# Kernel tuning notes

Hardware: AMD Instinct MI355X
Metric: run time of the kernel (lower is better)

The kernel has to match this reference:

```python
import jax, jax.numpy as jnp
import numpy as np

N = 50000      # nodes
E = 800000     # edges (avg degree 16)
IN = 128       # input feature dim
HID = 32       # per-head hidden dim
H = 4          # attention heads
C = 40         # num classes
SLOPE = 0.2    # leaky relu negative slope


def setup_inputs() -> dict:
    key = jax.random.key(0)
    ks = jax.random.split(key, 14)
    s = 0.05
    inputs = jax.random.normal(ks[0], (N, IN), jnp.float32)
    target = jax.random.normal(ks[1], (N, IN), jnp.float32)
    lamb = jax.random.uniform(ks[2], (1,), jnp.float32)
    src = jax.random.randint(ks[3], (E,), 0, N, jnp.int32)
    dst = jax.random.randint(ks[4], (E,), 0, N, jnp.int32)
    W0 = jax.random.normal(ks[5], (IN, H * HID), jnp.float32) * s
    al0 = jax.random.normal(ks[6], (H, HID), jnp.float32) * s
    ar0 = jax.random.normal(ks[7], (H, HID), jnp.float32) * s
    W1 = jax.random.normal(ks[8], (H * HID, H * HID), jnp.float32) * s
    al1 = jax.random.normal(ks[9], (H, HID), jnp.float32) * s
    ar1 = jax.random.normal(ks[10], (H, HID), jnp.float32) * s
    Wout = jax.random.normal(ks[11], (H * HID, C), jnp.float32) * s
    bout = jnp.zeros((C,), jnp.float32)
    return dict(inputs=inputs, target=target, lamb=lamb,
                W0=W0, al0=al0, ar0=ar0, W1=W1, al1=al1, ar1=ar1,
                Wout=Wout, bout=bout, src=src, dst=dst)


def gat_conv(h, W, al, ar, src, dst, residual):
    # h: [N, in_dim]; W: [in_dim, H*HID]; al/ar: [H, HID]
    feat = (h @ W).reshape(N, H, HID)                  # [N,H,D]
    el = jnp.einsum('nhd,hd->nh', feat, al)            # [N,H]
    er = jnp.einsum('nhd,hd->nh', feat, ar)            # [N,H]
    e = jax.nn.leaky_relu(el[src] + er[dst], SLOPE)    # [E,H]
    # edge softmax over incoming edges of each dst node
    emax = jax.ops.segment_max(e, dst, num_segments=N)  # [N,H]
    ee = jnp.exp(e - emax[dst])                          # [E,H]
    denom = jax.ops.segment_sum(ee, dst, num_segments=N)
    a = ee / denom[dst]                                  # [E,H]
    msg = feat[src] * a[:, :, None]                      # [E,H,D]
    out = jax.ops.segment_sum(msg, dst, num_segments=N)  # [N,H,D]
    if residual:
        out = out + h.reshape(N, H, HID)  # identity residual (in == H*HID)
    return jax.nn.elu(out)


def reference(inputs, target, lamb, W0, al0, ar0, W1, al1, ar1, Wout, bout, src, dst):
    def path(x):
        h = gat_conv(x, W0, al0, ar0, src, dst, residual=False).reshape(N, H * HID)
        h = gat_conv(h, W1, al1, ar1, src, dst, residual=True).reshape(N, H * HID)
        return h

    h = path(inputs)
    h2 = path(target)
    lam = lamb[0]
    h = lam * h + (1.0 - lam) * h2   # mixup_hidden=True
    logits = h @ Wout + bout
    return (h, logits)
```

## Files before the change

### kernel.cpp

```cpp
#include <hip/hip_runtime.h>
#include <hip/hip_bf16.h>
#include <cstddef>

#define GN 50000
#define GE 800000
#define GH 4
#define GD 32
#define SLOPE 0.2f
#define LOG2E 1.4426950408889634f

typedef unsigned short ushort_t;
typedef unsigned int uint_t;
using short8 = __attribute__((ext_vector_type(8))) short;
using float4v = __attribute__((ext_vector_type(4))) float;

__device__ __forceinline__ ushort_t f2bf(float f) {
    union { float f; uint_t u; } v; v.f = f;
    uint_t r = v.u + 0x7fff + ((v.u >> 16) & 1);
    return (ushort_t)(r >> 16);
}
__device__ __forceinline__ float bflo(uint_t u) { return __uint_as_float(u << 16); }
__device__ __forceinline__ float bfhi(uint_t u) { return __uint_as_float(u & 0xffff0000u); }
__device__ __forceinline__ float bfu(ushort_t u) { return __uint_as_float((uint_t)u << 16); }

__device__ __forceinline__ uint_t cvt_pk_bf16(float lo, float hi) {
    uint_t r;
    asm("v_cvt_pk_bf16_f32 %0, %1, %2" : "=v"(r) : "v"(lo), "v"(hi));
    return r;
}

#if __has_builtin(__builtin_amdgcn_exp2f)
#define EXP2F(x) __builtin_amdgcn_exp2f(x)
#else
#define EXP2F(x) exp2f(x)
#endif

__device__ __forceinline__ int slotmap(int a) {
    return (a < GN) ? (a << 1) : (((a - GN) << 1) | 1);
}

__global__ void k_hist(const int* __restrict__ dst, int* __restrict__ deg, int E) {
    int i = blockIdx.x * 256 + threadIdx.x;
    if (i < E) atomicAdd(&deg[dst[i]], 1);
}

__global__ void k_scan1(const int* __restrict__ deg, int* __restrict__ row_ptr,
                        int* __restrict__ partials, int n) {
    __shared__ int s[256];
    int t = threadIdx.x;
    int i = blockIdx.x * 256 + t;
    int v = (i < n) ? deg[i] : 0;
    s[t] = v;
    __syncthreads();
    for (int off = 1; off < 256; off <<= 1) {
        int add = (t >= off) ? s[t - off] : 0;
        __syncthreads();
        s[t] += add;
        __syncthreads();
    }
    if (i < n) row_ptr[i] = s[t] - v;
    if (t == 255) partials[blockIdx.x] = s[255];
}

__global__ void k_scan2(int* __restrict__ partials, int nb) {
    __shared__ int s[256];
    int t = threadIdx.x;
    int v = (t < nb) ? partials[t] : 0;
    s[t] = v;
    __syncthreads();
    for (int off = 1; off < 256; off <<= 1) {
        int add = (t >= off) ? s[t - off] : 0;
        __syncthreads();
        s[t] += add;
        __syncthreads();
    }
    if (t < nb) partials[t] = s[t] - v;
}

__global__ void k_scan3(int* __restrict__ row_ptr, int* __restrict__ wpos,
                        const int* __restrict__ partials, int n, int E) {
    int i = blockIdx.x * 256 + threadIdx.x;
    if (i < n) {
        int rp = row_ptr[i] + partials[i >> 8];
        row_ptr[i] = rp;
        wpos[i] = rp;
        if (i == 0) row_ptr[n] = E;
    }
}

__global__ void k_fill(const int* __restrict__ src, const int* __restrict__ dst,
                       int* __restrict__ wpos, int* __restrict__ csr_src, int E) {
    int i = blockIdx.x * 256 + threadIdx.x;
    if (i < E) {
        int p = atomicAdd(&wpos[dst[i]], 1);
        csr_src[p] = src[i];
    }
}

__global__ void k_cvt_all(const float* __restrict__ W0, const float* __restrict__ W1,
                          const float* __restrict__ Wout,
                          ushort_t* __restrict__ wbt, ushort_t* __restrict__ woutb) {
    int t = blockIdx.x * 256 + threadIdx.x;
    if (t < 32768) {
        int m = t >> 14;
        int o = t & 16383;
        int n = o >> 7, k = o & 127;
        const float* W = m ? W1 : W0;
        wbt[t] = f2bf(W[k * 128 + n]);
    } else {
        int u = t - 32768;
        if (u < 48 * 128) {
            int n = u >> 7, k = u & 127;
            float w = (n < 40) ? Wout[k * 40 + n] : 0.f;
            ushort_t h = f2bf(w);
            woutb[u] = h;
            woutb[48 * 128 + u] = f2bf(w - bfu(h));
        }
    }
}

__device__ __forceinline__ void lr_epilogue(const float4v acc[2][8],
                                            const float* __restrict__ ar,
                                            float* __restrict__ er,
                                            int r0, int quad, int col, int M) {
#pragma unroll
    for (int rt = 0; rt < 2; rt++) {
#pragma unroll
        for (int h = 0; h < 4; h++) {
            float arv0 = ar[h * 32 + col], arv1 = ar[h * 32 + 16 + col];
            float pr[4];
#pragma unroll
            for (int r = 0; r < 4; r++)
                pr[r] = acc[rt][2 * h][r] * arv0 + acc[rt][2 * h + 1][r] * arv1;
#pragma unroll
            for (int m = 1; m < 16; m <<= 1) {
#pragma unroll
                for (int r = 0; r < 4; r++) pr[r] += __shfl_xor(pr[r], m, 64);
            }
            if (col == 8 + h) {
#pragma unroll
                for (int r = 0; r < 4; r++) {
                    int row = r0 + rt * 16 + quad * 4 + r;
                    if (row < M) er[slotmap(row) * 4 + h] = pr[r] * LOG2E;
                }
            }
        }
    }
}

__device__ __forceinline__ void store_c_bf16(ushort_t* __restrict__ Cb,
                                             const float4v acc[2][8],
                                             int r0, int quad, int col, int M) {
#pragma unroll
    for (int rt = 0; rt < 2; rt++)
#pragma unroll
        for (int nt = 0; nt < 8; nt++) {
            int rb = r0 + rt * 16 + quad * 4;
            int c = nt * 16 + col;
            uint_t p01 = cvt_pk_bf16(acc[rt][nt][0], acc[rt][nt][1]);
            uint_t p23 = cvt_pk_bf16(acc[rt][nt][2], acc[rt][nt][3]);
            if (rb + 0 < M) Cb[(size_t)slotmap(rb + 0) * 128 + c] = (ushort_t)p01;
            if (rb + 1 < M) Cb[(size_t)slotmap(rb + 1) * 128 + c] = (ushort_t)(p01 >> 16);
            if (rb + 2 < M) Cb[(size_t)slotmap(rb + 2) * 128 + c] = (ushort_t)p23;
            if (rb + 3 < M) Cb[(size_t)slotmap(rb + 3) * 128 + c] = (ushort_t)(p23 >> 16);
        }
}

__global__ __launch_bounds__(256) void gemm_mfma32(const float* __restrict__ A0,
                                                   const float* __restrict__ A1,
                                                   const ushort_t* __restrict__ WbT,
                                                   const float* __restrict__ ar,
                                                   ushort_t* __restrict__ Cb,
                                                   float* __restrict__ er, int M) {
    __shared__ ushort_t Bs[128][136];
    int tid = threadIdx.x;
    for (int i = tid; i < 128 * 16; i += 256) {
        int n = i >> 4;
        int kc = (i & 15) << 3;
        *(short8*)&Bs[n][kc] = *(const short8*)&WbT[n * 128 + kc];
    }
    __syncthreads();
    int wid = tid >> 6, lane = tid & 63;
    int r0 = blockIdx.x * 128 + wid * 32;
    int col = lane & 15, quad = lane >> 4;
    float4v acc[2][8];
#pragma unroll
    for (int rt = 0; rt < 2; rt++)
#pragma unroll
        for (int t = 0; t < 8; t++) acc[rt][t] = (float4v){0.f, 0.f, 0.f, 0.f};
    int ar_[2] = {r0 + col, r0 + 16 + col};
    const float* Ap[2];
#pragma unroll
    for (int rt = 0; rt < 2; rt++) {
        int a = ar_[rt];
        Ap[rt] = (a < M) ? ((a < GN) ? (A0 + (size_t)a * 128)
                                     : (A1 + (size_t)(a - GN) * 128)) : nullptr;
    }
#pragma unroll
    for (int ks = 0; ks < 4; ks++) {
        short8 af[2];
#pragma unroll
        for (int rt = 0; rt < 2; rt++) {
            af[rt] = (short8){};
            if (Ap[rt]) {
                float4 v0 = *(const float4*)&Ap[rt][ks * 32 + quad * 8];
                float4 v1 = *(const float4*)&Ap[rt][ks * 32 + quad * 8 + 4];
                union { short8 s; uint_t u[4]; } cv;
                cv.u[0] = cvt_pk_bf16(v0.x, v0.y);
                cv.u[1] = cvt_pk_bf16(v0.z, v0.w);
                cv.u[2] = cvt_pk_bf16(v1.x, v1.y);
                cv.u[3] = cvt_pk_bf16(v1.z, v1.w);
                af[rt] = cv.s;
            }
        }
#pragma unroll
        for (int nt = 0; nt < 8; nt++) {
            short8 bf = *(const short8*)&Bs[nt * 16 + col][ks * 32 + quad * 8];
            acc[0][nt] = __builtin_amdgcn_mfma_f32_16x16x32_bf16(af[0], bf, acc[0][nt], 0, 0, 0);
            acc[1][nt] = __builtin_amdgcn_mfma_f32_16x16x32_bf16(af[1], bf, acc[1][nt], 0, 0, 0);
        }
    }
    store_c_bf16(Cb, acc, r0, quad, col, M);
    lr_epilogue(acc, ar, er, r0, quad, col, M);
}

__global__ __launch_bounds__(256) void gemm_mfma(const ushort_t* __restrict__ A,
                                                 const ushort_t* __restrict__ WbT,
                                                 const float* __restrict__ ar,
                                                 ushort_t* __restrict__ Cb,
                                                 float* __restrict__ er, int M) {
    __shared__ ushort_t Bs[128][136];
    int tid = threadIdx.x;
    for (int i = tid; i < 128 * 16; i += 256) {
        int n = i >> 4;
        int kc = (i & 15) << 3;
        *(short8*)&Bs[n][kc] = *(const short8*)&WbT[n * 128 + kc];
    }
    __syncthreads();
    int wid = tid >> 6, lane = tid & 63;
    int r0 = blockIdx.x * 128 + wid * 32;
    int col = lane & 15, quad = lane >> 4;
    float4v acc[2][8];
#pragma unroll
    for (int rt = 0; rt < 2; rt++)
#pragma unroll
        for (int t = 0; t < 8; t++) acc[rt][t] = (float4v){0.f, 0.f, 0.f, 0.f};
    int ar_[2] = {r0 + col, r0 + 16 + col};
    const ushort_t* Ap[2];
#pragma unroll
    for (int rt = 0; rt < 2; rt++) {
        int a = ar_[rt];
        Ap[rt] = (a < M) ? (A + (size_t)slotmap(a) * 128) : nullptr;
    }
#pragma unroll
    for (int ks = 0; ks < 4; ks++) {
        short8 af[2];
#pragma unroll
        for (int rt = 0; rt < 2; rt++) {
            af[rt] = (short8){};
            if (Ap[rt]) af[rt] = *(const short8*)&Ap[rt][ks * 32 + quad * 8];
        }
#pragma unroll
        for (int nt = 0; nt < 8; nt++) {
            short8 bf = *(const short8*)&Bs[nt * 16 + col][ks * 32 + quad * 8];
            acc[0][nt] = __builtin_amdgcn_mfma_f32_16x16x32_bf16(af[0], bf, acc[0][nt], 0, 0, 0);
            acc[1][nt] = __builtin_amdgcn_mfma_f32_16x16x32_bf16(af[1], bf, acc[1][nt], 0, 0, 0);
        }
    }
    store_c_bf16(Cb, acc, r0, quad, col, M);
    lr_epilogue(acc, ar, er, r0, quad, col, M);
}

__device__ __forceinline__ void agg_core(
    const ushort_t* __restrict__ featb, float4 alv, float ern,
    const int* __restrict__ csr_src, int base, int deg, uint_t fofs,
    float& v0, float& v1, float& v2, float& v3) {
    if (deg <= 0) { v0 = v1 = v2 = v3 = 0.f; return; }
    float a0 = 0.f, a1 = 0.f, a2 = 0.f, a3 = 0.f, ss = 0.f;
    int nblk = (deg + 15) >> 4;
    int jb = base;
    int r1 = deg - 1;
    int s[16], t[16];
#pragma unroll
    for (int k = 0; k < 16; k++) s[k] = csr_src[jb + min(k, r1)];
    int b = 0;
    for (;;) {
        int rem = deg - (b << 4);
        uint2 f[16];
#pragma unroll
        for (int k = 0; k < 16; k++)
            f[k] = *(const uint2*)&featb[(uint_t)s[k] * 256u + fofs];
        bool more = (b + 1) < nblk;
        if (more) {
            int nj = jb + 16;
            int r2 = rem - 17;
#pragma unroll
            for (int k = 0; k < 16; k++) t[k] = csr_src[nj + min(k, r2)];
        }
#pragma unroll
        for (int k = 0; k < 16; k++) {
            float x0 = bflo(f[k].x), x1 = bfhi(f[k].x);
            float x2 = bflo(f[k].y), x3 = bfhi(f[k].y);
            float d = x0 * alv.x + x1 * alv.y + x2 * alv.z + x3 * alv.w;
            d += __shfl_xor(d, 1, 64);
            d += __shfl_xor(d, 2, 64);
            d += __shfl_xor(d, 4, 64);
            float e = d + ern;
            e = fmaxf(e, SLOPE * e);
            float w = (k < rem) ? EXP2F(e) : 0.f;
            ss += w;
            a0 += w * x0; a1 += w * x1; a2 += w * x2; a3 += w * x3;
        }
        if (!more) break;
        b++; jb += 16;
#pragma unroll
        for (int k = 0; k < 16; k++) s[k] = t[k];
    }
    float inv = 1.f / ss;
    v0 = a0 * inv; v1 = a1 * inv; v2 = a2 * inv; v3 = a3 * inv;
}

__global__ __launch_bounds__(512) void gat_agg_l1(
    const ushort_t* __restrict__ featb, const float* __restrict__ al,
    const float* __restrict__ er, const int* __restrict__ row_ptr,
    const int* __restrict__ csr_src, ushort_t* __restrict__ abuf) {
    int n = __builtin_amdgcn_readfirstlane(blockIdx.x * 8 + (threadIdx.x >> 6));
    if (n >= GN) return;
    int lane = threadIdx.x & 63;
    int half = lane >> 5;
    int q = lane & 31;
    int head = (lane >> 3) & 3, j8 = lane & 7, q4 = q << 2;
    float4 alv = *(const float4*)&al[head * 32 + j8 * 4];
    alv.x *= LOG2E; alv.y *= LOG2E; alv.z *= LOG2E; alv.w *= LOG2E;
    uint_t fofs = (uint_t)(half * 128 + q4);
    float ern = er[(uint_t)n * 8u + (uint_t)(half * 4 + head)];
    int base = row_ptr[n];
    int deg = row_ptr[n + 1] - base;
    float v0, v1, v2, v3;
    agg_core(featb, alv, ern, csr_src, base, deg, fofs, v0, v1, v2, v3);
    v0 = v0 > 0.f ? v0 : __expf(v0) - 1.f;
    v1 = v1 > 0.f ? v1 : __expf(v1) - 1.f;
    v2 = v2 > 0.f ? v2 : __expf(v2) - 1.f;
    v3 = v3 > 0.f ? v3 : __expf(v3) - 1.f;
    size_t idx = ((size_t)(2 * n + half)) * 128 + q4;
    uint2 o;
    o.x = cvt_pk_bf16(v0, v1);
    o.y = cvt_pk_bf16(v2, v3);
    *(uint2*)&abuf[idx] = o;
}

__global__ __launch_bounds__(512) void gat_agg_l2(
    const ushort_t* __restrict__ featb, const float* __restrict__ al,
    const float* __restrict__ er, const int* __restrict__ row_ptr,
    const int* __restrict__ csr_src, const ushort_t* __restrict__ resid,
    const float* __restrict__ lamb, float* __restrict__ outh) {
    int tid = threadIdx.x;
    int n = __builtin_amdgcn_readfirstlane(blockIdx.x * 8 + (tid >> 6));
    if (n >= GN) return;
    int lane = tid & 63;
    int half = lane >> 5;
    int q = lane & 31;
    int head = (lane >> 3) & 3, j8 = lane & 7, q4 = q << 2;
    float4 alv = *(const float4*)&al[head * 32 + j8 * 4];
    alv.x *= LOG2E; alv.y *= LOG2E; alv.z *= LOG2E; alv.w *= LOG2E;
    uint_t fofs = (uint_t)(half * 128 + q4);
    float ern = er[(uint_t)n * 8u + (uint_t)(half * 4 + head)];
    int base = row_ptr[n];
    int deg = row_ptr[n + 1] - base;
    float v0, v1, v2, v3;
    agg_core(featb, alv, ern, csr_src, base, deg, fofs, v0, v1, v2, v3);
    size_t idx = ((size_t)(2 * n + half)) * 128 + q4;
    ushort4 r = *(const ushort4*)&resid[idx];
    v0 += bfu(r.x); v1 += bfu(r.y); v2 += bfu(r.z); v3 += bfu(r.w);
    v0 = v0 > 0.f ? v0 : __expf(v0) - 1.f;
    v1 = v1 > 0.f ? v1 : __expf(v1) - 1.f;
    v2 = v2 > 0.f ? v2 : __expf(v2) - 1.f;
    v3 = v3 > 0.f ? v3 : __expf(v3) - 1.f;
    float p0 = __shfl_xor(v0, 32, 64);
    float p1 = __shfl_xor(v1, 32, 64);
    float p2 = __shfl_xor(v2, 32, 64);
    float p3 = __shfl_xor(v3, 32, 64);
    float lam = lamb[0];
    if (half == 0) {
        float m0 = lam * v0 + (1.f - lam) * p0;
        float m1 = lam * v1 + (1.f - lam) * p1;
        float m2 = lam * v2 + (1.f - lam) * p2;
        float m3 = lam * v3 + (1.f - lam) * p3;
        *(float4*)&outh[(size_t)n * 128 + q4] = make_float4(m0, m1, m2, m3);
    }
}

__global__ __launch_bounds__(256) void k_logits(const float* __restrict__ Hf,
                                                const ushort_t* __restrict__ Wb,
                                                const float* __restrict__ bout,
                                                float* __restrict__ outlog) {
    __shared__ ushort_t Bh[48][136];
    __shared__ ushort_t Bl[48][136];
    int tid = threadIdx.x;
    for (int i = tid; i < 48 * 16; i += 256) {
        int n = i >> 4;
        int kc = (i & 15) << 3;
        *(short8*)&Bh[n][kc] = *(const short8*)&Wb[n * 128 + kc];
        *(short8*)&Bl[n][kc] = *(const short8*)&Wb[48 * 128 + n * 128 + kc];
    }
    __syncthreads();
    int wid = tid >> 6, lane = tid & 63;
    int r0 = blockIdx.x * 128 + wid * 32;
    int col = lane & 15, quad = lane >> 4;
    float4v acc[2][3];
#pragma unroll
    for (int rt = 0; rt < 2; rt++)
#pragma unroll
        for (int nt = 0; nt < 3; nt++) acc[rt][nt] = (float4v){0.f, 0.f, 0.f, 0.f};
    int ar_[2] = {r0 + col, r0 + 16 + col};
#pragma unroll
    for (int ks = 0; ks < 4; ks++) {
        short8 ah[2], alo[2];
#pragma unroll
        for (int rt = 0; rt < 2; rt++) {
            ah[rt] = (short8){};
            alo[rt] = (short8){};
            if (ar_[rt] < GN) {
                const float* p = Hf + (size_t)ar_[rt] * 128 + ks * 32 + quad * 8;
                float4 x = *(const float4*)p;
                float4 y = *(const float4*)(p + 4);
                union { short8 s; uint_t u[4]; } ch, cl;
                ch.u[0] = cvt_pk_bf16(x.x, x.y);
                ch.u[1] = cvt_pk_bf16(x.z, x.w);
                ch.u[2] = cvt_pk_bf16(y.x, y.y);
                ch.u[3] = cvt_pk_bf16(y.z, y.w);
                cl.u[0] = cvt_pk_bf16(x.x - bflo(ch.u[0]), x.y - bfhi(ch.u[0]));
                cl.u[1] = cvt_pk_bf16(x.z - bflo(ch.u[1]), x.w - bfhi(ch.u[1]));
                cl.u[2] = cvt_pk_bf16(y.x - bflo(ch.u[2]), y.y - bfhi(ch.u[2]));
                cl.u[3] = cvt_pk_bf16(y.z - bflo(ch.u[3]), y.w - bfhi(ch.u[3]));
                ah[rt] = ch.s;
                alo[rt] = cl.s;
            }
        }
#pragma unroll
        for (int nt = 0; nt < 3; nt++) {
            short8 bh = *(const short8*)&Bh[nt * 16 + col][ks * 32 + quad * 8];
            short8 bl = *(const short8*)&Bl[nt * 16 + col][ks * 32 + quad * 8];
#pragma unroll
            for (int rt = 0; rt < 2; rt++) {
                acc[rt][nt] = __builtin_amdgcn_mfma_f32_16x16x32_bf16(ah[rt], bh, acc[rt][nt], 0, 0, 0);
                acc[rt][nt] = __builtin_amdgcn_mfma_f32_16x16x32_bf16(alo[rt], bh, acc[rt][nt], 0, 0, 0);
                acc[rt][nt] = __builtin_amdgcn_mfma_f32_16x16x32_bf16(ah[rt], bl, acc[rt][nt], 0, 0, 0);
            }
        }
    }
#pragma unroll
    for (int nt = 0; nt < 3; nt++) {
        int c = nt * 16 + col;
        if (c < 40) {
            float bv = bout[c];
#pragma unroll
            for (int rt = 0; rt < 2; rt++)
#pragma unroll
                for (int r = 0; r < 4; r++) {
                    int row = r0 + rt * 16 + quad * 4 + r;
                    if (row < GN) outlog[(size_t)row * 40 + c] = acc[rt][nt][r] + bv;
                }
        }
    }
}

extern "C" void kernel_launch(void* const* d_in, const int* in_sizes, int n_in,
                              void* d_out, int out_size, void* d_ws, size_t ws_size,
                              hipStream_t stream) {
    const float* inputs = (const float*)d_in[0];
    const float* target = (const float*)d_in[1];
    const float* lamb   = (const float*)d_in[2];
    const float* W0     = (const float*)d_in[3];
    const float* al0    = (const float*)d_in[4];
    const float* ar0    = (const float*)d_in[5];
    const float* W1     = (const float*)d_in[6];
    const float* al1    = (const float*)d_in[7];
    const float* ar1    = (const float*)d_in[8];
    const float* Wout   = (const float*)d_in[9];
    const float* bout   = (const float*)d_in[10];
    const int*   src    = (const int*)d_in[11];
    const int*   dst    = (const int*)d_in[12];

    float* out = (float*)d_out;
    float* outh = out;
    float* outlog = out + (size_t)GN * 128;

    const int NP = 2 * GN;
    ushort_t* featb = (ushort_t*)d_ws;
    ushort_t* abuf  = featb + (size_t)NP * 128;
    float* er = (float*)(abuf + (size_t)NP * 128);
    ushort_t* wbt = (ushort_t*)(er + (size_t)NP * GH);
    int* row_ptr  = (int*)(wbt + 2 * 128 * 128);
    int* wpos     = row_ptr + (GN + 1);
    int* csr_src  = wpos + GN;
    int* partials = csr_src + GE + 16;
    ushort_t* woutb = (ushort_t*)(partials + 256);

    const int nb = (GN + 255) / 256;
    const int eb = (GE + 255) / 256;
    const int gblocks = (NP + 127) / 128;
    const int aggblocks = (GN + 7) / 8;
    const int lblocks = (GN + 127) / 128;

    hipMemsetAsync(wpos, 0, GN * sizeof(int), stream);
    k_hist<<<eb, 256, 0, stream>>>(dst, wpos, GE);
    k_scan1<<<nb, 256, 0, stream>>>(wpos, row_ptr, partials, GN);
    k_scan2<<<1, 256, 0, stream>>>(partials, nb);
    k_scan3<<<nb, 256, 0, stream>>>(row_ptr, wpos, partials, GN, GE);
    k_fill<<<eb, 256, 0, stream>>>(src, dst, wpos, csr_src, GE);

    k_cvt_all<<<152, 256, 0, stream>>>(W0, W1, Wout, wbt, woutb);

    gemm_mfma32<<<gblocks, 256, 0, stream>>>(inputs, target, wbt, ar0,
                                             featb, er, NP);
    gat_agg_l1<<<aggblocks, 512, 0, stream>>>(featb, al0, er, row_ptr, csr_src, abuf);

    gemm_mfma<<<gblocks, 256, 0, stream>>>(abuf, wbt + 128 * 128, ar1,
                                           featb, er, NP);
    gat_agg_l2<<<aggblocks, 512, 0, stream>>>(featb, al1, er, row_ptr, csr_src,
                                              abuf, lamb, outh);

    k_logits<<<lblocks, 256, 0, stream>>>(outh, woutb, bout, outlog);
}
```

Before: 396.5 us.

## Precompute el in GEMM epilogue and stream edges across eight nodes per wave

The GEMM epilogue now also computes the left attention scores el per node, so aggregation reads a precomputed scalar per edge instead of recomputing a 32-wide dot product with shuffles for every edge. The aggregation kernel is rewritten so each wave walks a contiguous run of edges covering eight destination nodes in fixed windows of eight. A new per-edge csr_dst array supplies the destination index, and edge weights are spread across lanes with ds_swizzle. This is meant to cut per-edge ALU and shuffle work and the padding waste of low-degree nodes, in exchange for an extra el buffer, the csr_dst writes and more complex control flow at node boundaries.

```diff
diff --git a/kernel.cpp b/kernel.cpp
--- a/kernel.cpp
+++ b/kernel.cpp
@@ -34,6 +34,8 @@
 #else
 #define EXP2F(x) exp2f(x)
 #endif
+
+#define SWZ_B(v, imm) __uint_as_float((uint_t)__builtin_amdgcn_ds_swizzle((int)__float_as_uint(v), (imm)))
 
 __device__ __forceinline__ int slotmap(int a) {
     return (a < GN) ? (a << 1) : (((a - GN) << 1) | 1);
@@ -89,11 +91,14 @@
 }
 
 __global__ void k_fill(const int* __restrict__ src, const int* __restrict__ dst,
-                       int* __restrict__ wpos, int* __restrict__ csr_src, int E) {
+                       int* __restrict__ wpos, int* __restrict__ csr_src,
+                       ushort_t* __restrict__ csr_dst, int E) {
     int i = blockIdx.x * 256 + threadIdx.x;
     if (i < E) {
-        int p = atomicAdd(&wpos[dst[i]], 1);
+        int d = dst[i];
+        int p = atomicAdd(&wpos[d], 1);
         csr_src[p] = src[i];
+        csr_dst[p] = (ushort_t)d;
     }
 }
 
@@ -120,22 +125,37 @@
 }
 
 __device__ __forceinline__ void lr_epilogue(const float4v acc[2][8],
+                                            const float* __restrict__ al,
                                             const float* __restrict__ ar,
+                                            float* __restrict__ el,
                                             float* __restrict__ er,
                                             int r0, int quad, int col, int M) {
 #pragma unroll
     for (int rt = 0; rt < 2; rt++) {
 #pragma unroll
         for (int h = 0; h < 4; h++) {
+            float alv0 = al[h * 32 + col], alv1 = al[h * 32 + 16 + col];
             float arv0 = ar[h * 32 + col], arv1 = ar[h * 32 + 16 + col];
-            float pr[4];
-#pragma unroll
-            for (int r = 0; r < 4; r++)
+            float pl[4], pr[4];
+#pragma unroll
+            for (int r = 0; r < 4; r++) {
+                pl[r] = acc[rt][2 * h][r] * alv0 + acc[rt][2 * h + 1][r] * alv1;
                 pr[r] = acc[rt][2 * h][r] * arv0 + acc[rt][2 * h + 1][r] * arv1;
+            }
 #pragma unroll
             for (int m = 1; m < 16; m <<= 1) {
 #pragma unroll
-                for (int r = 0; r < 4; r++) pr[r] += __shfl_xor(pr[r], m, 64);
+                for (int r = 0; r < 4; r++) {
+                    pl[r] += __shfl_xor(pl[r], m, 64);
+                    pr[r] += __shfl_xor(pr[r], m, 64);
+                }
+            }
+            if (col == h) {
+#pragma unroll
+                for (int r = 0; r < 4; r++) {
+                    int row = r0 + rt * 16 + quad * 4 + r;
+                    if (row < M) el[slotmap(row) * 4 + h] = pl[r] * LOG2E;
+                }
             }
             if (col == 8 + h) {
 #pragma unroll
@@ -169,8 +189,10 @@
 __global__ __launch_bounds__(256) void gemm_mfma32(const float* __restrict__ A0,
                                                    const float* __restrict__ A1,
                                                    const ushort_t* __restrict__ WbT,
+                                                   const float* __restrict__ al,
                                                    const float* __restrict__ ar,
                                                    ushort_t* __restrict__ Cb,
+                                                   float* __restrict__ el,
                                                    float* __restrict__ er, int M) {
     __shared__ ushort_t Bs[128][136];
     int tid = threadIdx.x;
@@ -221,13 +243,15 @@
         }
     }
     store_c_bf16(Cb, acc, r0, quad, col, M);
-    lr_epilogue(acc, ar, er, r0, quad, col, M);
+    lr_epilogue(acc, al, ar, el, er, r0, quad, col, M);
 }
 
 __global__ __launch_bounds__(256) void gemm_mfma(const ushort_t* __restrict__ A,
                                                  const ushort_t* __restrict__ WbT,
+                                                 const float* __restrict__ al,
                                                  const float* __restrict__ ar,
                                                  ushort_t* __restrict__ Cb,
+                                                 float* __restrict__ el,
                                                  float* __restrict__ er, int M) {
     __shared__ ushort_t Bs[128][136];
     int tid = threadIdx.x;
@@ -268,125 +292,142 @@
         }
     }
     store_c_bf16(Cb, acc, r0, quad, col, M);
-    lr_epilogue(acc, ar, er, r0, quad, col, M);
-}
-
-__device__ __forceinline__ void agg_core(
-    const ushort_t* __restrict__ featb, float4 alv, float ern,
-    const int* __restrict__ csr_src, int base, int deg, uint_t fofs,
-    float& v0, float& v1, float& v2, float& v3) {
-    if (deg <= 0) { v0 = v1 = v2 = v3 = 0.f; return; }
+    lr_epilogue(acc, al, ar, el, er, r0, quad, col, M);
+}
+
+template<int MODE>
+__global__ __launch_bounds__(512) void gat_agg_stream(
+    const ushort_t* __restrict__ featb, const float* __restrict__ el,
+    const float* __restrict__ er, const int* __restrict__ row_ptr,
+    const int* __restrict__ csr_src, const ushort_t* __restrict__ csr_dst,
+    const ushort_t* __restrict__ resid, const float* __restrict__ lamb,
+    ushort_t* __restrict__ abuf, float* __restrict__ outh) {
+    int tid = threadIdx.x;
+    int n0 = __builtin_amdgcn_readfirstlane((blockIdx.x * 8 + (tid >> 6)) * 8);
+    if (n0 >= GN) return;
+    int nn = min(8, GN - n0);
+    int lane = tid & 63;
+    int half = lane >> 5, q = lane & 31;
+    int lk = lane & 7, q4 = q << 2;
+    uint_t eo = (uint_t)(half * 4 + ((lane >> 3) & 3));
+    uint_t fofs = (uint_t)(half * 128 + q4);
+    int start = row_ptr[n0];
+    int end = row_ptr[n0 + nn];
+    int cn = 0;
+    int cur_end = row_ptr[n0 + min(1, nn)];
+    int nxt_end = row_ptr[n0 + min(2, nn)];
+    float lam = (MODE == 1) ? lamb[0] : 0.f;
     float a0 = 0.f, a1 = 0.f, a2 = 0.f, a3 = 0.f, ss = 0.f;
-    int nblk = (deg + 15) >> 4;
-    int jb = base;
-    int r1 = deg - 1;
-    int s[16], t[16];
-#pragma unroll
-    for (int k = 0; k < 16; k++) s[k] = csr_src[jb + min(k, r1)];
-    int b = 0;
-    for (;;) {
-        int rem = deg - (b << 4);
-        uint2 f[16];
-#pragma unroll
-        for (int k = 0; k < 16; k++)
-            f[k] = *(const uint2*)&featb[(uint_t)s[k] * 256u + fofs];
-        bool more = (b + 1) < nblk;
-        if (more) {
-            int nj = jb + 16;
-            int r2 = rem - 17;
-#pragma unroll
-            for (int k = 0; k < 16; k++) t[k] = csr_src[nj + min(k, r2)];
-        }
-#pragma unroll
-        for (int k = 0; k < 16; k++) {
-            float x0 = bflo(f[k].x), x1 = bfhi(f[k].x);
-            float x2 = bflo(f[k].y), x3 = bfhi(f[k].y);
-            float d = x0 * alv.x + x1 * alv.y + x2 * alv.z + x3 * alv.w;
-            d += __shfl_xor(d, 1, 64);
-            d += __shfl_xor(d, 2, 64);
-            d += __shfl_xor(d, 4, 64);
-            float e = d + ern;
+    uint2 rnx = make_uint2(0u, 0u);
+    if (MODE == 1) rnx = *(const uint2*)&resid[((size_t)(2 * n0 + half)) * 128 + q4];
+
+    auto finalize = [&]() {
+        float inv = (ss > 0.f) ? 1.f / ss : 0.f;
+        float v0 = a0 * inv, v1 = a1 * inv, v2 = a2 * inv, v3 = a3 * inv;
+        if (MODE == 1) {
+            uint2 rc = rnx;
+            int nx = n0 + min(cn + 1, nn - 1);
+            rnx = *(const uint2*)&resid[((size_t)(2 * nx + half)) * 128 + q4];
+            v0 += bflo(rc.x); v1 += bfhi(rc.x); v2 += bflo(rc.y); v3 += bfhi(rc.y);
+        }
+        v0 = v0 > 0.f ? v0 : __expf(v0) - 1.f;
+        v1 = v1 > 0.f ? v1 : __expf(v1) - 1.f;
+        v2 = v2 > 0.f ? v2 : __expf(v2) - 1.f;
+        v3 = v3 > 0.f ? v3 : __expf(v3) - 1.f;
+        if (MODE == 0) {
+            uint2 o;
+            o.x = cvt_pk_bf16(v0, v1);
+            o.y = cvt_pk_bf16(v2, v3);
+            *(uint2*)&abuf[((size_t)(2 * (n0 + cn) + half)) * 128 + q4] = o;
+        } else {
+            float p0 = __shfl_xor(v0, 32, 64);
+            float p1 = __shfl_xor(v1, 32, 64);
+            float p2 = __shfl_xor(v2, 32, 64);
+            float p3 = __shfl_xor(v3, 32, 64);
+            if (half == 0) {
+                *(float4*)&outh[(size_t)(n0 + cn) * 128 + q4] =
+                    make_float4(lam * v0 + (1.f - lam) * p0,
+                                lam * v1 + (1.f - lam) * p1,
+                                lam * v2 + (1.f - lam) * p2,
+                                lam * v3 + (1.f - lam) * p3);
+            }
+        }
+        a0 = a1 = a2 = a3 = ss = 0.f;
+    };
+
+    int nwin = (end - start + 7) >> 3;
+    if (nwin > 0) {
+        int e1 = end - 1;
+        int sw[8], tw[8];
+        int j = start;
+#pragma unroll
+        for (int k = 0; k < 8; k++) sw[k] = csr_src[min(j + k, e1)];
+        int pA = min(j + lk, e1);
+        int sA = csr_src[pA];
+        int dA = (int)csr_dst[pA];
+        float elA = el[(uint_t)sA * 8u + eo];
+        float erA = er[(uint_t)dA * 8u + eo];
+        uint2 fc[8], fn[8];
+#pragma unroll
+        for (int k = 0; k < 8; k++)
+            fc[k] = *(const uint2*)&featb[(uint_t)sw[k] * 256u + fofs];
+        for (int b = 0;;) {
+            bool more = (b + 1) < nwin;
+            int sB = 0, dB = 0;
+            float elB = 0.f, erB = 0.f;
+            if (more) {
+                int nj = j + 8;
+#pragma unroll
+                for (int k = 0; k < 8; k++) tw[k] = csr_src[min(nj + k, e1)];
+                int pB = min(nj + lk, e1);
+                sB = csr_src[pB];
+                dB = (int)csr_dst[pB];
+                elB = el[(uint_t)sB * 8u + eo];
+                erB = er[(uint_t)dB * 8u + eo];
+            }
+            float e = elA + erA;
             e = fmaxf(e, SLOPE * e);
-            float w = (k < rem) ? EXP2F(e) : 0.f;
-            ss += w;
-            a0 += w * x0; a1 += w * x1; a2 += w * x2; a3 += w * x3;
-        }
-        if (!more) break;
-        b++; jb += 16;
-#pragma unroll
-        for (int k = 0; k < 16; k++) s[k] = t[k];
-    }
-    float inv = 1.f / ss;
-    v0 = a0 * inv; v1 = a1 * inv; v2 = a2 * inv; v3 = a3 * inv;
-}
-
-__global__ __launch_bounds__(512) void gat_agg_l1(
-    const ushort_t* __restrict__ featb, const float* __restrict__ al,
-    const float* __restrict__ er, const int* __restrict__ row_ptr,
-    const int* __restrict__ csr_src, ushort_t* __restrict__ abuf) {
-    int n = __builtin_amdgcn_readfirstlane(blockIdx.x * 8 + (threadIdx.x >> 6));
-    if (n >= GN) return;
-    int lane = threadIdx.x & 63;
-    int half = lane >> 5;
-    int q = lane & 31;
-    int head = (lane >> 3) & 3, j8 = lane & 7, q4 = q << 2;
-    float4 alv = *(const float4*)&al[head * 32 + j8 * 4];
-    alv.x *= LOG2E; alv.y *= LOG2E; alv.z *= LOG2E; alv.w *= LOG2E;
-    uint_t fofs = (uint_t)(half * 128 + q4);
-    float ern = er[(uint_t)n * 8u + (uint_t)(half * 4 + head)];
-    int base = row_ptr[n];
-    int deg = row_ptr[n + 1] - base;
-    float v0, v1, v2, v3;
-    agg_core(featb, alv, ern, csr_src, base, deg, fofs, v0, v1, v2, v3);
-    v0 = v0 > 0.f ? v0 : __expf(v0) - 1.f;
-    v1 = v1 > 0.f ? v1 : __expf(v1) - 1.f;
-    v2 = v2 > 0.f ? v2 : __expf(v2) - 1.f;
-    v3 = v3 > 0.f ? v3 : __expf(v3) - 1.f;
-    size_t idx = ((size_t)(2 * n + half)) * 128 + q4;
-    uint2 o;
-    o.x = cvt_pk_bf16(v0, v1);
-    o.y = cvt_pk_bf16(v2, v3);
-    *(uint2*)&abuf[idx] = o;
-}
-
-__global__ __launch_bounds__(512) void gat_agg_l2(
-    const ushort_t* __restrict__ featb, const float* __restrict__ al,
-    const float* __restrict__ er, const int* __restrict__ row_ptr,
-    const int* __restrict__ csr_src, const ushort_t* __restrict__ resid,
-    const float* __restrict__ lamb, float* __restrict__ outh) {
-    int tid = threadIdx.x;
-    int n = __builtin_amdgcn_readfirstlane(blockIdx.x * 8 + (tid >> 6));
-    if (n >= GN) return;
-    int lane = tid & 63;
-    int half = lane >> 5;
-    int q = lane & 31;
-    int head = (lane >> 3) & 3, j8 = lane & 7, q4 = q << 2;
-    float4 alv = *(const float4*)&al[head * 32 + j8 * 4];
-    alv.x *= LOG2E; alv.y *= LOG2E; alv.z *= LOG2E; alv.w *= LOG2E;
-    uint_t fofs = (uint_t)(half * 128 + q4);
-    float ern = er[(uint_t)n * 8u + (uint_t)(half * 4 + head)];
-    int base = row_ptr[n];
-    int deg = row_ptr[n + 1] - base;
-    float v0, v1, v2, v3;
-    agg_core(featb, alv, ern, csr_src, base, deg, fofs, v0, v1, v2, v3);
-    size_t idx = ((size_t)(2 * n + half)) * 128 + q4;
-    ushort4 r = *(const ushort4*)&resid[idx];
-    v0 += bfu(r.x); v1 += bfu(r.y); v2 += bfu(r.z); v3 += bfu(r.w);
-    v0 = v0 > 0.f ? v0 : __expf(v0) - 1.f;
-    v1 = v1 > 0.f ? v1 : __expf(v1) - 1.f;
-    v2 = v2 > 0.f ? v2 : __expf(v2) - 1.f;
-    v3 = v3 > 0.f ? v3 : __expf(v3) - 1.f;
-    float p0 = __shfl_xor(v0, 32, 64);
-    float p1 = __shfl_xor(v1, 32, 64);
-    float p2 = __shfl_xor(v2, 32, 64);
-    float p3 = __shfl_xor(v3, 32, 64);
-    float lam = lamb[0];
-    if (half == 0) {
-        float m0 = lam * v0 + (1.f - lam) * p0;
-        float m1 = lam * v1 + (1.f - lam) * p1;
-        float m2 = lam * v2 + (1.f - lam) * p2;
-        float m3 = lam * v3 + (1.f - lam) * p3;
-        *(float4*)&outh[(size_t)n * 128 + q4] = make_float4(m0, m1, m2, m3);
+            float wown = EXP2F(e);
+            if (more) {
+#pragma unroll
+                for (int k = 0; k < 8; k++)
+                    fn[k] = *(const uint2*)&featb[(uint_t)tw[k] * 256u + fofs];
+            }
+            float wv[8];
+            wv[0] = SWZ_B(wown, 0x018);
+            wv[1] = SWZ_B(wown, 0x038);
+            wv[2] = SWZ_B(wown, 0x058);
+            wv[3] = SWZ_B(wown, 0x078);
+            wv[4] = SWZ_B(wown, 0x098);
+            wv[5] = SWZ_B(wown, 0x0B8);
+            wv[6] = SWZ_B(wown, 0x0D8);
+            wv[7] = SWZ_B(wown, 0x0F8);
+#pragma unroll
+            for (int k = 0; k < 8; k++) {
+                int eid = j + k;
+                while (eid == cur_end && cn < nn) {
+                    finalize();
+                    cn++;
+                    cur_end = nxt_end;
+                    nxt_end = row_ptr[n0 + min(cn + 2, nn)];
+                }
+                if (eid >= end) break;
+                float w = wv[k];
+                float x0 = bflo(fc[k].x), x1 = bfhi(fc[k].x);
+                float x2 = bflo(fc[k].y), x3 = bfhi(fc[k].y);
+                ss += w;
+                a0 += w * x0; a1 += w * x1; a2 += w * x2; a3 += w * x3;
+            }
+            if (!more) break;
+            b++; j += 8;
+#pragma unroll
+            for (int k = 0; k < 8; k++) { sw[k] = tw[k]; fc[k] = fn[k]; }
+            sA = sB; dA = dB; elA = elB; erA = erB;
+        }
+    }
+    while (cn < nn) {
+        finalize();
+        cn++;
     }
 }
 
@@ -489,18 +530,20 @@
     const int NP = 2 * GN;
     ushort_t* featb = (ushort_t*)d_ws;
     ushort_t* abuf  = featb + (size_t)NP * 128;
-    float* er = (float*)(abuf + (size_t)NP * 128);
+    float* el = (float*)(abuf + (size_t)NP * 128);
+    float* er = el + (size_t)NP * GH;
     ushort_t* wbt = (ushort_t*)(er + (size_t)NP * GH);
     int* row_ptr  = (int*)(wbt + 2 * 128 * 128);
     int* wpos     = row_ptr + (GN + 1);
     int* csr_src  = wpos + GN;
-    int* partials = csr_src + GE + 16;
+    ushort_t* csr_dst = (ushort_t*)(csr_src + GE + 16);
+    int* partials = (int*)(csr_dst + GE + 16);
     ushort_t* woutb = (ushort_t*)(partials + 256);
 
     const int nb = (GN + 255) / 256;
     const int eb = (GE + 255) / 256;
     const int gblocks = (NP + 127) / 128;
-    const int aggblocks = (GN + 7) / 8;
+    const int aggblocks = (GN + 63) / 64;
     const int lblocks = (GN + 127) / 128;
 
     hipMemsetAsync(wpos, 0, GN * sizeof(int), stream);
@@ -508,18 +551,21 @@
     k_scan1<<<nb, 256, 0, stream>>>(wpos, row_ptr, partials, GN);
     k_scan2<<<1, 256, 0, stream>>>(partials, nb);
     k_scan3<<<nb, 256, 0, stream>>>(row_ptr, wpos, partials, GN, GE);
-    k_fill<<<eb, 256, 0, stream>>>(src, dst, wpos, csr_src, GE);
+    k_fill<<<eb, 256, 0, stream>>>(src, dst, wpos, csr_src, csr_dst, GE);
 
     k_cvt_all<<<152, 256, 0, stream>>>(W0, W1, Wout, wbt, woutb);
 
-    gemm_mfma32<<<gblocks, 256, 0, stream>>>(inputs, target, wbt, ar0,
-                                             featb, er, NP);
-    gat_agg_l1<<<aggblocks, 512, 0, stream>>>(featb, al0, er, row_ptr, csr_src, abuf);
-
-    gemm_mfma<<<gblocks, 256, 0, stream>>>(abuf, wbt + 128 * 128, ar1,
-                                           featb, er, NP);
-    gat_agg_l2<<<aggblocks, 512, 0, stream>>>(featb, al1, er, row_ptr, csr_src,
-                                              abuf, lamb, outh);
+    gemm_mfma32<<<gblocks, 256, 0, stream>>>(inputs, target, wbt, al0, ar0,
+                                             featb, el, er, NP);
+    gat_agg_stream<0><<<aggblocks, 512, 0, stream>>>(featb, el, er, row_ptr,
+                                                     csr_src, csr_dst, nullptr,
+                                                     nullptr, abuf, nullptr);
+
+    gemm_mfma<<<gblocks, 256, 0, stream>>>(abuf, wbt + 128 * 128, al1, ar1,
+                                           featb, el, er, NP);
+    gat_agg_stream<1><<<aggblocks, 512, 0, stream>>>(featb, el, er, row_ptr,
+                                                     csr_src, csr_dst, abuf,
+                                                     lamb, nullptr, outh);
 
     k_logits<<<lblocks, 256, 0, stream>>>(outh, woutb, bout, outlog);
 }
```

New measurement: 444.7 us. 1.12x slower.

## Precompute per-node source attention logits in GEMM epilogue instead of per-edge dot

Applied to the files above, without the earlier changes.

The GEMM epilogue now also computes el (feature·al per head) and stores it per node, alongside er. The aggregation kernels no longer recompute the per-edge dot product with shuffle reductions. Instead each lane gathers el for up to two edges per 16-edge block, computes the exp weights once, and broadcasts them with ds_swizzle. This removes redundant per-edge arithmetic and cross-lane traffic in the hot gather loop, at the cost of extra el gathers and epilogue work. It also changes rounding slightly, since el is now computed from the fp32 accumulator rather than from bf16 features.

```diff
diff --git a/kernel.cpp b/kernel.cpp
--- a/kernel.cpp
+++ b/kernel.cpp
@@ -34,6 +34,8 @@
 #else
 #define EXP2F(x) exp2f(x)
 #endif
+
+#define SWZ_B(v, imm) __uint_as_float((uint_t)__builtin_amdgcn_ds_swizzle((int)__float_as_uint(v), (imm)))
 
 __device__ __forceinline__ int slotmap(int a) {
     return (a < GN) ? (a << 1) : (((a - GN) << 1) | 1);
@@ -120,22 +122,37 @@
 }
 
 __device__ __forceinline__ void lr_epilogue(const float4v acc[2][8],
+                                            const float* __restrict__ al,
                                             const float* __restrict__ ar,
+                                            float* __restrict__ el,
                                             float* __restrict__ er,
                                             int r0, int quad, int col, int M) {
 #pragma unroll
     for (int rt = 0; rt < 2; rt++) {
 #pragma unroll
         for (int h = 0; h < 4; h++) {
+            float alv0 = al[h * 32 + col], alv1 = al[h * 32 + 16 + col];
             float arv0 = ar[h * 32 + col], arv1 = ar[h * 32 + 16 + col];
-            float pr[4];
-#pragma unroll
-            for (int r = 0; r < 4; r++)
+            float pl[4], pr[4];
+#pragma unroll
+            for (int r = 0; r < 4; r++) {
+                pl[r] = acc[rt][2 * h][r] * alv0 + acc[rt][2 * h + 1][r] * alv1;
                 pr[r] = acc[rt][2 * h][r] * arv0 + acc[rt][2 * h + 1][r] * arv1;
+            }
 #pragma unroll
             for (int m = 1; m < 16; m <<= 1) {
 #pragma unroll
-                for (int r = 0; r < 4; r++) pr[r] += __shfl_xor(pr[r], m, 64);
+                for (int r = 0; r < 4; r++) {
+                    pl[r] += __shfl_xor(pl[r], m, 64);
+                    pr[r] += __shfl_xor(pr[r], m, 64);
+                }
+            }
+            if (col == h) {
+#pragma unroll
+                for (int r = 0; r < 4; r++) {
+                    int row = r0 + rt * 16 + quad * 4 + r;
+                    if (row < M) el[slotmap(row) * 4 + h] = pl[r] * LOG2E;
+                }
             }
             if (col == 8 + h) {
 #pragma unroll
@@ -169,8 +186,10 @@
 __global__ __launch_bounds__(256) void gemm_mfma32(const float* __restrict__ A0,
                                                    const float* __restrict__ A1,
                                                    const ushort_t* __restrict__ WbT,
+                                                   const float* __restrict__ al,
                                                    const float* __restrict__ ar,
                                                    ushort_t* __restrict__ Cb,
+                                                   float* __restrict__ el,
                                                    float* __restrict__ er, int M) {
     __shared__ ushort_t Bs[128][136];
     int tid = threadIdx.x;
@@ -221,13 +240,15 @@
         }
     }
     store_c_bf16(Cb, acc, r0, quad, col, M);
-    lr_epilogue(acc, ar, er, r0, quad, col, M);
+    lr_epilogue(acc, al, ar, el, er, r0, quad, col, M);
 }
 
 __global__ __launch_bounds__(256) void gemm_mfma(const ushort_t* __restrict__ A,
                                                  const ushort_t* __restrict__ WbT,
+                                                 const float* __restrict__ al,
                                                  const float* __restrict__ ar,
                                                  ushort_t* __restrict__ Cb,
+                                                 float* __restrict__ el,
                                                  float* __restrict__ er, int M) {
     __shared__ ushort_t Bs[128][136];
     int tid = threadIdx.x;
@@ -268,60 +289,72 @@
         }
     }
     store_c_bf16(Cb, acc, r0, quad, col, M);
-    lr_epilogue(acc, ar, er, r0, quad, col, M);
+    lr_epilogue(acc, al, ar, el, er, r0, quad, col, M);
 }
 
 __device__ __forceinline__ void agg_core(
-    const ushort_t* __restrict__ featb, float4 alv, float ern,
-    const int* __restrict__ csr_src, int base, int deg, uint_t fofs,
-    float& v0, float& v1, float& v2, float& v3) {
+    const ushort_t* __restrict__ featb, const float* __restrict__ el, float ern,
+    const int* __restrict__ csr_src, int base, int deg, uint_t eo, uint_t fofs,
+    int lk, float& v0, float& v1, float& v2, float& v3) {
     if (deg <= 0) { v0 = v1 = v2 = v3 = 0.f; return; }
     float a0 = 0.f, a1 = 0.f, a2 = 0.f, a3 = 0.f, ss = 0.f;
     int nblk = (deg + 15) >> 4;
+    int e1 = base + deg - 1;
     int jb = base;
-    int r1 = deg - 1;
     int s[16], t[16];
 #pragma unroll
-    for (int k = 0; k < 16; k++) s[k] = csr_src[jb + min(k, r1)];
-    int b = 0;
-    for (;;) {
+    for (int k = 0; k < 16; k++) s[k] = csr_src[min(jb + k, e1)];
+    float elA = el[(uint_t)csr_src[min(jb + lk, e1)] * 8u + eo];
+    float elB = el[(uint_t)csr_src[min(jb + lk + 8, e1)] * 8u + eo];
+    for (int b = 0;;) {
         int rem = deg - (b << 4);
         uint2 f[16];
 #pragma unroll
         for (int k = 0; k < 16; k++)
             f[k] = *(const uint2*)&featb[(uint_t)s[k] * 256u + fofs];
         bool more = (b + 1) < nblk;
+        float elA2 = 0.f, elB2 = 0.f;
         if (more) {
             int nj = jb + 16;
-            int r2 = rem - 17;
-#pragma unroll
-            for (int k = 0; k < 16; k++) t[k] = csr_src[nj + min(k, r2)];
-        }
+#pragma unroll
+            for (int k = 0; k < 16; k++) t[k] = csr_src[min(nj + k, e1)];
+            elA2 = el[(uint_t)csr_src[min(nj + lk, e1)] * 8u + eo];
+            elB2 = el[(uint_t)csr_src[min(nj + lk + 8, e1)] * 8u + eo];
+        }
+        float eA = elA + ern; eA = fmaxf(eA, SLOPE * eA);
+        float eB = elB + ern; eB = fmaxf(eB, SLOPE * eB);
+        float wA = (lk < rem) ? EXP2F(eA) : 0.f;
+        float wB = (lk + 8 < rem) ? EXP2F(eB) : 0.f;
+        float wv[16];
+        wv[0]  = SWZ_B(wA, 0x018); wv[1]  = SWZ_B(wA, 0x038);
+        wv[2]  = SWZ_B(wA, 0x058); wv[3]  = SWZ_B(wA, 0x078);
+        wv[4]  = SWZ_B(wA, 0x098); wv[5]  = SWZ_B(wA, 0x0B8);
+        wv[6]  = SWZ_B(wA, 0x0D8); wv[7]  = SWZ_B(wA, 0x0F8);
+        wv[8]  = SWZ_B(wB, 0x018); wv[9]  = SWZ_B(wB, 0x038);
+        wv[10] = SWZ_B(wB, 0x058); wv[11] = SWZ_B(wB, 0x078);
+        wv[12] = SWZ_B(wB, 0x098); wv[13] = SWZ_B(wB, 0x0B8);
+        wv[14] = SWZ_B(wB, 0x0D8); wv[15] = SWZ_B(wB, 0x0F8);
 #pragma unroll
         for (int k = 0; k < 16; k++) {
-            float x0 = bflo(f[k].x), x1 = bfhi(f[k].x);
-            float x2 = bflo(f[k].y), x3 = bfhi(f[k].y);
-            float d = x0 * alv.x + x1 * alv.y + x2 * alv.z + x3 * alv.w;
-            d += __shfl_xor(d, 1, 64);
-            d += __shfl_xor(d, 2, 64);
-            d += __shfl_xor(d, 4, 64);
-            float e = d + ern;
-            e = fmaxf(e, SLOPE * e);
-            float w = (k < rem) ? EXP2F(e) : 0.f;
+            float w = wv[k];
             ss += w;
-            a0 += w * x0; a1 += w * x1; a2 += w * x2; a3 += w * x3;
+            a0 += w * bflo(f[k].x);
+            a1 += w * bfhi(f[k].x);
+            a2 += w * bflo(f[k].y);
+            a3 += w * bfhi(f[k].y);
         }
         if (!more) break;
         b++; jb += 16;
 #pragma unroll
         for (int k = 0; k < 16; k++) s[k] = t[k];
+        elA = elA2; elB = elB2;
     }
     float inv = 1.f / ss;
     v0 = a0 * inv; v1 = a1 * inv; v2 = a2 * inv; v3 = a3 * inv;
 }
 
 __global__ __launch_bounds__(512) void gat_agg_l1(
-    const ushort_t* __restrict__ featb, const float* __restrict__ al,
+    const ushort_t* __restrict__ featb, const float* __restrict__ el,
     const float* __restrict__ er, const int* __restrict__ row_ptr,
     const int* __restrict__ csr_src, ushort_t* __restrict__ abuf) {
     int n = __builtin_amdgcn_readfirstlane(blockIdx.x * 8 + (threadIdx.x >> 6));
@@ -329,15 +362,14 @@
     int lane = threadIdx.x & 63;
     int half = lane >> 5;
     int q = lane & 31;
-    int head = (lane >> 3) & 3, j8 = lane & 7, q4 = q << 2;
-    float4 alv = *(const float4*)&al[head * 32 + j8 * 4];
-    alv.x *= LOG2E; alv.y *= LOG2E; alv.z *= LOG2E; alv.w *= LOG2E;
+    int lk = lane & 7, q4 = q << 2;
+    uint_t eo = (uint_t)(half * 4 + ((lane >> 3) & 3));
     uint_t fofs = (uint_t)(half * 128 + q4);
-    float ern = er[(uint_t)n * 8u + (uint_t)(half * 4 + head)];
+    float ern = er[(uint_t)n * 8u + eo];
     int base = row_ptr[n];
     int deg = row_ptr[n + 1] - base;
     float v0, v1, v2, v3;
-    agg_core(featb, alv, ern, csr_src, base, deg, fofs, v0, v1, v2, v3);
+    agg_core(featb, el, ern, csr_src, base, deg, eo, fofs, lk, v0, v1, v2, v3);
     v0 = v0 > 0.f ? v0 : __expf(v0) - 1.f;
     v1 = v1 > 0.f ? v1 : __expf(v1) - 1.f;
     v2 = v2 > 0.f ? v2 : __expf(v2) - 1.f;
@@ -350,7 +382,7 @@
 }
 
 __global__ __launch_bounds__(512) void gat_agg_l2(
-    const ushort_t* __restrict__ featb, const float* __restrict__ al,
+    const ushort_t* __restrict__ featb, const float* __restrict__ el,
     const float* __restrict__ er, const int* __restrict__ row_ptr,
     const int* __restrict__ csr_src, const ushort_t* __restrict__ resid,
     const float* __restrict__ lamb, float* __restrict__ outh) {
@@ -360,15 +392,14 @@
     int lane = tid & 63;
     int half = lane >> 5;
     int q = lane & 31;
-    int head = (lane >> 3) & 3, j8 = lane & 7, q4 = q << 2;
-    float4 alv = *(const float4*)&al[head * 32 + j8 * 4];
-    alv.x *= LOG2E; alv.y *= LOG2E; alv.z *= LOG2E; alv.w *= LOG2E;
+    int lk = lane & 7, q4 = q << 2;
+    uint_t eo = (uint_t)(half * 4 + ((lane >> 3) & 3));
     uint_t fofs = (uint_t)(half * 128 + q4);
-    float ern = er[(uint_t)n * 8u + (uint_t)(half * 4 + head)];
+    float ern = er[(uint_t)n * 8u + eo];
     int base = row_ptr[n];
     int deg = row_ptr[n + 1] - base;
     float v0, v1, v2, v3;
-    agg_core(featb, alv, ern, csr_src, base, deg, fofs, v0, v1, v2, v3);
+    agg_core(featb, el, ern, csr_src, base, deg, eo, fofs, lk, v0, v1, v2, v3);
     size_t idx = ((size_t)(2 * n + half)) * 128 + q4;
     ushort4 r = *(const ushort4*)&resid[idx];
     v0 += bfu(r.x); v1 += bfu(r.y); v2 += bfu(r.z); v3 += bfu(r.w);
@@ -489,7 +520,8 @@
     const int NP = 2 * GN;
     ushort_t* featb = (ushort_t*)d_ws;
     ushort_t* abuf  = featb + (size_t)NP * 128;
-    float* er = (float*)(abuf + (size_t)NP * 128);
+    float* el = (float*)(abuf + (size_t)NP * 128);
+    float* er = el + (size_t)NP * GH;
     ushort_t* wbt = (ushort_t*)(er + (size_t)NP * GH);
     int* row_ptr  = (int*)(wbt + 2 * 128 * 128);
     int* wpos     = row_ptr + (GN + 1);
@@ -512,13 +544,13 @@
 
     k_cvt_all<<<152, 256, 0, stream>>>(W0, W1, Wout, wbt, woutb);
 
-    gemm_mfma32<<<gblocks, 256, 0, stream>>>(inputs, target, wbt, ar0,
-                                             featb, er, NP);
-    gat_agg_l1<<<aggblocks, 512, 0, stream>>>(featb, al0, er, row_ptr, csr_src, abuf);
-
-    gemm_mfma<<<gblocks, 256, 0, stream>>>(abuf, wbt + 128 * 128, ar1,
-                                           featb, er, NP);
-    gat_agg_l2<<<aggblocks, 512, 0, stream>>>(featb, al1, er, row_ptr, csr_src,
+    gemm_mfma32<<<gblocks, 256, 0, stream>>>(inputs, target, wbt, al0, ar0,
+                                             featb, el, er, NP);
+    gat_agg_l1<<<aggblocks, 512, 0, stream>>>(featb, el, er, row_ptr, csr_src, abuf);
+
+    gemm_mfma<<<gblocks, 256, 0, stream>>>(abuf, wbt + 128 * 128, al1, ar1,
+                                           featb, el, er, NP);
+    gat_agg_l2<<<aggblocks, 512, 0, stream>>>(featb, el, er, row_ptr, csr_src,
                                               abuf, lamb, outh);
 
     k_logits<<<lblocks, 256, 0, stream>>>(outh, woutb, bout, outlog);
```

Measured after the change: 406.9 us. +2.6%, slower.
